# Optimization experiments

Hardware: AMD Instinct MI355X
Metric: run time of the kernel (lower is better)

## Reference

```python
import jax, jax.numpy as jnp
import numpy as np

B, T, DIN, DH, A = 2048, 32, 1024, 64, 64
EPS = 1e-12  # tf.contrib.layers.layer_norm variance epsilon


def _ln(x, g, b, axes):
    mu = jnp.mean(x, axes, keepdims=True)
    var = jnp.var(x, axes, keepdims=True)
    return (x - mu) / jnp.sqrt(var + EPS) * g + b


def _lstm(x_seq, W, b, H):
    # BasicLSTMCell: z = [x, h] @ W + b ; gates in order i, j, f, o ; forget_bias=1.0
    def step(carry, xt):
        c, h = carry
        z = jnp.concatenate([xt, h], axis=-1) @ W + b
        i, j, f, o = jnp.split(z, 4, axis=-1)
        c = c * jax.nn.sigmoid(f + 1.0) + jax.nn.sigmoid(i) * jnp.tanh(j)
        h = jnp.tanh(c) * jax.nn.sigmoid(o)
        return (c, h), h
    Bb = x_seq.shape[0]
    init = (jnp.zeros((Bb, H), x_seq.dtype), jnp.zeros((Bb, H), x_seq.dtype))
    _, hs = jax.lax.scan(step, init, jnp.swapaxes(x_seq, 0, 1))  # [T,B,H]
    return jnp.swapaxes(hs, 0, 1)  # [B,T,H]


def _revseq(x, lens):
    # tf.reverse_sequence along time axis 1
    t = jnp.arange(x.shape[1])[None, :]
    idx = jnp.where(t < lens[:, None], lens[:, None] - 1 - t, t)
    return jnp.take_along_axis(x, idx[:, :, None], axis=1)


def setup_inputs() -> dict:
    key = jax.random.key(0)
    ks = jax.random.split(key, 8)
    H = 512
    s_d = 1.0 / np.sqrt(DIN)
    s_l = 1.0 / np.sqrt(DH + H)
    return {
        "ud": jax.random.normal(ks[0], (B * T, DIN), jnp.float32),
        "mask": jnp.ones((B, T), jnp.float32),
        "au": jax.random.randint(ks[1], (B,), 1, T + 1, jnp.int32),
        "n_hidden": H,
        "ln1_g": jnp.ones((DIN,), jnp.float32),
        "ln1_b": jnp.zeros((DIN,), jnp.float32),
        "W_dense": jax.random.normal(ks[2], (DIN, DH), jnp.float32) * s_d,
        "b_dense": jnp.zeros((DH,), jnp.float32),
        "ln2_g": jnp.ones((DH,), jnp.float32),
        "ln2_b": jnp.zeros((DH,), jnp.float32),
        "W_fw": jax.random.normal(ks[3], (DH + H, 4 * H), jnp.float32) * s_l,
        "b_fw": jnp.zeros((4 * H,), jnp.float32),
        "W_bw": jax.random.normal(ks[4], (DH + H, 4 * H), jnp.float32) * s_l,
        "b_bw": jnp.zeros((4 * H,), jnp.float32),
        "ln3_g": jnp.ones((2 * H,), jnp.float32),
        "ln3_b": jnp.zeros((2 * H,), jnp.float32),
        "W_conv": jax.random.uniform(ks[5], (2 * H, A), jnp.float32, -0.003, 0.003),
        "b_conv": jnp.zeros((A,), jnp.float32),
    }


def reference(ud, mask, au, n_hidden, ln1_g, ln1_b, W_dense, b_dense, ln2_g, ln2_b,
              W_fw, b_fw, W_bw, b_bw, ln3_g, ln3_b, W_conv, b_conv):
    H = n_hidden
    x = _ln(ud, ln1_g, ln1_b, -1)                     # [B*T, DIN]
    x = x @ W_dense + b_dense                          # [B*T, DH]
    x = jax.nn.relu(_ln(x, ln2_g, ln2_b, -1))
    x = x.reshape(B, T, DH)
    tmask = (jnp.arange(T)[None, :] < au[:, None]).astype(x.dtype)  # [B,T]
    fw = _lstm(x, W_fw, b_fw, H) * tmask[:, :, None]
    bw = _revseq(_lstm(_revseq(x, au), W_bw, b_bw, H) * tmask[:, :, None], au)
    h = jnp.concatenate([fw, bw], axis=-1)             # [B,T,2H]
    # contrib layer_norm: begin_norm_axis=1 -> normalize over (T, 2H) jointly
    h = jax.nn.relu(_ln(h, ln3_g, ln3_b, (1, 2)))
    # conv1d kernel_size=stride=2H on [B, T*2H, 1] == per-timestep matmul
    out = jnp.tanh(jnp.einsum('bth,ha->bta', h, W_conv) + b_conv)  # [B,T,A]
    return out
```

## Files before the change

kernel.cpp:

```cpp
#include <hip/hip_runtime.h>

#define B_   2048
#define T_   32
#define DIN_ 1024
#define DH_  64
#define H_   512
#define KL_  576
#define AO_  64

typedef unsigned short u16;
typedef unsigned int   u32;
typedef __attribute__((ext_vector_type(8))) short          bf16x8;
typedef __attribute__((ext_vector_type(8))) unsigned short u16x8;
typedef __attribute__((ext_vector_type(4))) float          f32x4;

__device__ __forceinline__ u16 f2bf(float f) {
  u32 u = __builtin_bit_cast(u32, f);
  u = (u + 0x7FFFu + ((u >> 16) & 1u)) >> 16;
  return (u16)u;
}
__device__ __forceinline__ float bf2f(u16 s) {
  return __builtin_bit_cast(float, (u32)s << 16);
}
__device__ __forceinline__ float sigm(float x) { return 1.f / (1.f + __expf(-x)); }
__device__ __forceinline__ float tanh_(float x) { return 1.f - 2.f / (__expf(2.f * x) + 1.f); }

__device__ __forceinline__ void gl_lds16(const void* g, void* l) {
  __builtin_amdgcn_global_load_lds((const __attribute__((address_space(1))) u32*)g,
                                   (__attribute__((address_space(3))) u32*)l, 16, 0, 0);
}

__global__ __launch_bounds__(256) void k_transpose(const float* __restrict__ src,
                                                   u16* __restrict__ dst, int K, int N) {
  __shared__ float t[32][33];
  const int n0 = blockIdx.x * 32, k0 = blockIdx.y * 32;
  const int a = threadIdx.x >> 5, b = threadIdx.x & 31;
#pragma unroll
  for (int i = 0; i < 4; ++i)
    t[a + 8 * i][b] = src[(size_t)(k0 + a + 8 * i) * N + n0 + b];
  __syncthreads();
#pragma unroll
  for (int i = 0; i < 4; ++i)
    dst[(size_t)(n0 + a + 8 * i) * K + k0 + b] = f2bf(t[b][a + 8 * i]);
}

__global__ void k_gw(const float* __restrict__ W, const float* __restrict__ g,
                     const float* __restrict__ b, float* __restrict__ gW,
                     float* __restrict__ bW) {
  const int n = threadIdx.x;
  float sg = 0.f, sb = 0.f;
  for (int k = 0; k < DIN_; ++k) {
    const float w = W[k * DH_ + n];
    sg += g[k] * w; sb += b[k] * w;
  }
  gW[n] = sg; bW[n] = sb;
}

__global__ __launch_bounds__(256) void k_front(
    const float* __restrict__ ud, const float* __restrict__ g1,
    const u16* __restrict__ Wdt, const float* __restrict__ gW,
    const float* __restrict__ bW, const float* __restrict__ bd,
    const float* __restrict__ g2, const float* __restrict__ b2,
    u16* __restrict__ xout) {
  __shared__ u16 lA[64 * 32];
  __shared__ u16 lB[64 * 32];
  __shared__ float smu[64], srs[64];
  const int tid = threadIdx.x, wave = tid >> 6, lane = tid & 63;
  const int m0 = blockIdx.x * 64;
  const int arow = tid >> 2, ach = tid & 3;
  const float* __restrict__ udp = ud + (size_t)(m0 + arow) * DIN_ + ach * 8;
  const float* __restrict__ g1p = g1 + ach * 8;
  const int cB = wave * 16 + (lane >> 2);
  const u16* __restrict__ wdp = Wdt + (size_t)cB * DIN_ + (lane & 3) * 8;
  u16* const lBb = &lB[wave * 512];
  u16x8* const lAp = (u16x8*)&lA[arow * 32 + ach * 8];
  const int quad = lane >> 4, col = lane & 15;

  float sx = 0.f, sxx = 0.f;
  f32x4 acc[4] = {};
  for (int kt = 0; kt < 32; ++kt) {
    const int k0 = kt * 32;
    __syncthreads();
    const float4 v0 = *(const float4*)(udp + k0);
    const float4 v1 = *(const float4*)(udp + k0 + 4);
    const float4 ga = *(const float4*)(g1p + k0);
    const float4 gb = *(const float4*)(g1p + k0 + 4);
    sx  += v0.x + v0.y + v0.z + v0.w + v1.x + v1.y + v1.z + v1.w;
    sxx += v0.x * v0.x + v0.y * v0.y + v0.z * v0.z + v0.w * v0.w
         + v1.x * v1.x + v1.y * v1.y + v1.z * v1.z + v1.w * v1.w;
    u16x8 pk;
    pk[0] = f2bf(v0.x * ga.x); pk[1] = f2bf(v0.y * ga.y);
    pk[2] = f2bf(v0.z * ga.z); pk[3] = f2bf(v0.w * ga.w);
    pk[4] = f2bf(v1.x * gb.x); pk[5] = f2bf(v1.y * gb.y);
    pk[6] = f2bf(v1.z * gb.z); pk[7] = f2bf(v1.w * gb.w);
    *lAp = pk;
    gl_lds16(wdp + k0, lBb);
    __syncthreads();
    const bf16x8 af = *(const bf16x8*)&lA[(wave * 16 + col) * 32 + quad * 8];
#pragma unroll
    for (int nt = 0; nt < 4; ++nt) {
      const bf16x8 bfr = *(const bf16x8*)&lB[(nt * 16 + col) * 32 + quad * 8];
      acc[nt] = __builtin_amdgcn_mfma_f32_16x16x32_bf16(af, bfr, acc[nt], 0, 0, 0);
    }
  }
  sx  += __shfl_xor(sx, 1);  sx  += __shfl_xor(sx, 2);
  sxx += __shfl_xor(sxx, 1); sxx += __shfl_xor(sxx, 2);
  if ((lane & 3) == 0) {
    const float mu = sx * (1.f / DIN_);
    const float var = sxx * (1.f / DIN_) - mu * mu;
    smu[arow] = mu;
    srs[arow] = rsqrtf(var + 1e-12f);
  }
  __syncthreads();
  float gwv[4], bwv[4], g2v[4], b2v[4];
#pragma unroll
  for (int nt = 0; nt < 4; ++nt) {
    const int n = nt * 16 + col;
    gwv[nt] = gW[n]; bwv[nt] = bW[n] + bd[n]; g2v[nt] = g2[n]; b2v[nt] = b2[n];
  }
#pragma unroll
  for (int r = 0; r < 4; ++r) {
    const int rl = wave * 16 + quad * 4 + r;
    const float mu = smu[rl], rs = srs[rl];
    float y[4]; float s1 = 0.f, s2 = 0.f;
#pragma unroll
    for (int nt = 0; nt < 4; ++nt) {
      y[nt] = rs * (acc[nt][r] - mu * gwv[nt]) + bwv[nt];
      s1 += y[nt]; s2 += y[nt] * y[nt];
    }
    s1 += __shfl_xor(s1, 1); s1 += __shfl_xor(s1, 2);
    s1 += __shfl_xor(s1, 4); s1 += __shfl_xor(s1, 8);
    s2 += __shfl_xor(s2, 1); s2 += __shfl_xor(s2, 2);
    s2 += __shfl_xor(s2, 4); s2 += __shfl_xor(s2, 8);
    const float mu2 = s1 * (1.f / 64.f);
    const float rs2 = rsqrtf(s2 * (1.f / 64.f) - mu2 * mu2 + 1e-12f);
    const size_t R = m0 + rl;
#pragma unroll
    for (int nt = 0; nt < 4; ++nt) {
      const float v = fmaxf((y[nt] - mu2) * rs2 * g2v[nt] + b2v[nt], 0.f);
      xout[R * 64 + nt * 16 + col] = f2bf(v);
    }
  }
}

__global__ __launch_bounds__(256) void k_step(
    const int s, const u16* __restrict__ x, const u16* __restrict__ Wt,
    const float* __restrict__ bfw, const float* __restrict__ bbw,
    const int* __restrict__ au, u16* __restrict__ hstate,
    float* __restrict__ cstate, u16* __restrict__ hout) {
  __shared__ u16 lA[2][128 * 64];
  __shared__ u16 lB[2][128 * 64];
  const int tid = threadIdx.x, wave = tid >> 6, lane = tid & 63;
  const int dir = blockIdx.z;
  const int m0 = blockIdx.x * 128;
  const int u0 = blockIdx.y * 32;
  const int rb = s & 1, wb = rb ^ 1;
  const u16* __restrict__ Wtd = Wt + (size_t)dir * 2048 * KL_;
  const float* __restrict__ bias = dir ? bbw : bfw;

  const int lrow = lane >> 3;
  const int kk = ((lane & 7) ^ lrow) * 8;
  const int ch0 = 2 * wave, ch1 = ch0 + 1;

  const u16* gx[4]; const u16* gh[2]; const u16* gB[2];
#pragma unroll
  for (int i = 0; i < 2; ++i) {
    const int ch = ch0 + i;
#pragma unroll
    for (int h = 0; h < 2; ++h) {
      const int b = m0 + ch * 16 + h * 8 + lrow;
      const int aub = au[b];
      const int tin = (dir == 0) ? s : ((s < aub) ? (aub - 1 - s) : s);
      gx[i * 2 + h] = x + ((size_t)b * T_ + tin) * DH_ + kk;
    }
    const int b0 = m0 + ch * 16 + lrow;
    gh[i] = hstate + (((size_t)dir * 2 + rb) * B_ + b0) * H_ + kk;
    const int n = 512 * (ch & 3) + u0 + ((ch >> 2) << 4) + lrow;
    gB[i] = Wtd + (size_t)n * KL_ + kk;
  }

  gl_lds16(gx[0], &lA[0][ch0 * 1024]);
  gl_lds16(gx[1], &lA[0][ch0 * 1024 + 512]);
  gl_lds16(gx[2], &lA[0][ch1 * 1024]);
  gl_lds16(gx[3], &lA[0][ch1 * 1024 + 512]);
  gl_lds16(gB[0],           &lB[0][ch0 * 1024]);
  gl_lds16(gB[0] + 8 * KL_, &lB[0][ch0 * 1024 + 512]);
  gl_lds16(gB[1],           &lB[0][ch1 * 1024]);
  gl_lds16(gB[1] + 8 * KL_, &lB[0][ch1 * 1024 + 512]);
  __syncthreads();

  f32x4 acc[4][4] = {};
  const int wm = wave >> 1, wn = wave & 1, quad = lane >> 4, col = lane & 15;
  const int swz = (col & 7) << 4;

  int cur = 0;
  for (int kt = 0; kt < 9; ++kt) {
    if (kt < 8) {
      const int nb = cur ^ 1;
      const int kh = kt * 64;
      gl_lds16(gh[0] + kh,          &lA[nb][ch0 * 1024]);
      gl_lds16(gh[0] + kh + 8 * H_, &lA[nb][ch0 * 1024 + 512]);
      gl_lds16(gh[1] + kh,          &lA[nb][ch1 * 1024]);
      gl_lds16(gh[1] + kh + 8 * H_, &lA[nb][ch1 * 1024 + 512]);
      gl_lds16(gB[0] + kh + 64,            &lB[nb][ch0 * 1024]);
      gl_lds16(gB[0] + kh + 64 + 8 * KL_,  &lB[nb][ch0 * 1024 + 512]);
      gl_lds16(gB[1] + kh + 64,            &lB[nb][ch1 * 1024]);
      gl_lds16(gB[1] + kh + 64 + 8 * KL_,  &lB[nb][ch1 * 1024 + 512]);
    }
    const char* la = (const char*)&lA[cur][0];
    const char* lb = (const char*)&lB[cur][0];
#pragma unroll
    for (int ks = 0; ks < 2; ++ks) {
      const int bko = (ks * 64 + quad * 16) ^ swz;
      bf16x8 bfrag[4];
#pragma unroll
      for (int nt = 0; nt < 4; ++nt)
        bfrag[nt] = *(const bf16x8*)(lb + (wn * 64 + nt * 16 + col) * 128 + bko);
#pragma unroll
      for (int mt = 0; mt < 4; ++mt) {
        const bf16x8 afrag = *(const bf16x8*)(la + (wm * 64 + mt * 16 + col) * 128 + bko);
#pragma unroll
        for (int nt = 0; nt < 4; ++nt)
          acc[mt][nt] = __builtin_amdgcn_mfma_f32_16x16x32_bf16(afrag, bfrag[nt], acc[mt][nt], 0, 0, 0);
      }
    }
    __syncthreads();
    cur ^= 1;
  }

  const int u = u0 + wn * 16 + col;
  const float bi = bias[u], bj = bias[512 + u], bff = bias[1024 + u], bo = bias[1536 + u];
#pragma unroll
  for (int mt = 0; mt < 4; ++mt) {
#pragma unroll
    for (int r = 0; r < 4; ++r) {
      const int brow = m0 + wm * 64 + mt * 16 + quad * 4 + r;
      const size_t ci = ((size_t)dir * B_ + brow) * H_ + u;
      const float zi = acc[mt][0][r] + bi;
      const float zj = acc[mt][1][r] + bj;
      const float zf = acc[mt][2][r] + bff;
      const float zo = acc[mt][3][r] + bo;
      const float cn = cstate[ci] * sigm(zf + 1.f) + sigm(zi) * tanh_(zj);
      const float hn = tanh_(cn) * sigm(zo);
      cstate[ci] = cn;
      hstate[(((size_t)dir * 2 + wb) * B_ + brow) * H_ + u] = f2bf(hn);
      const int aub = au[brow];
      const bool valid = (s < aub);
      const int pos = (dir == 0) ? s : (valid ? (aub - 1 - s) : s);
      const float val = valid ? hn : 0.f;
      hout[((size_t)brow * T_ + pos) * 1024 + (dir ? 512 : 0) + u] = f2bf(val);
    }
  }
}

__global__ __launch_bounds__(256) void k_ln3stats(const u16* __restrict__ hout,
                                                  float* __restrict__ st) {
  const int b = blockIdx.x, tid = threadIdx.x;
  const uint4* __restrict__ p = (const uint4*)(hout + (size_t)b * T_ * 1024);
  float sx = 0.f, sxx = 0.f;
  for (int j = tid; j < 4096; j += 256) {
    const uint4 q = p[j];
    const u32 w[4] = {q.x, q.y, q.z, q.w};
#pragma unroll
    for (int e = 0; e < 4; ++e) {
      const float a = bf2f((u16)(w[e] & 0xffff));
      const float c = bf2f((u16)(w[e] >> 16));
      sx += a + c; sxx += a * a + c * c;
    }
  }
#pragma unroll
  for (int m = 1; m < 64; m <<= 1) { sx += __shfl_xor(sx, m); sxx += __shfl_xor(sxx, m); }
  __shared__ float rs_[4], rq_[4];
  if ((tid & 63) == 0) { rs_[tid >> 6] = sx; rq_[tid >> 6] = sxx; }
  __syncthreads();
  if (tid == 0) {
    const float a = rs_[0] + rs_[1] + rs_[2] + rs_[3];
    const float c = rq_[0] + rq_[1] + rq_[2] + rq_[3];
    const float mu = a / 32768.f;
    const float var = c / 32768.f - mu * mu;
    st[b * 2] = mu; st[b * 2 + 1] = rsqrtf(var + 1e-12f);
  }
}

__global__ __launch_bounds__(256) void k_final(
    const u16* __restrict__ hin, const float* __restrict__ st,
    const float* __restrict__ g3, const float* __restrict__ b3,
    const u16* __restrict__ Wct, const float* __restrict__ bc,
    float* __restrict__ out) {
  __shared__ u16 lA[64 * 32];
  __shared__ u16 lB[64 * 32];
  const int tid = threadIdx.x, wave = tid >> 6, lane = tid & 63;
  const int m0 = blockIdx.x * 64;
  const int arow = tid >> 2, ach = tid & 3;
  const size_t R = m0 + arow;
  const float mu = st[(R >> 5) * 2], rs = st[(R >> 5) * 2 + 1];
  const u16* __restrict__ hp = hin + R * 1024 + ach * 8;
  const float* __restrict__ g3p = g3 + ach * 8;
  const float* __restrict__ b3p = b3 + ach * 8;
  const int cB = wave * 16 + (lane >> 2);
  const u16* __restrict__ wcp = Wct + (size_t)cB * DIN_ + (lane & 3) * 8;
  u16* const lBb = &lB[wave * 512];
  u16x8* const lAp = (u16x8*)&lA[arow * 32 + ach * 8];
  const int quad = lane >> 4, col = lane & 15;
  f32x4 acc[4] = {};
  for (int kt = 0; kt < 32; ++kt) {
    const int k0 = kt * 32;
    __syncthreads();
    const uint4 q = *(const uint4*)(hp + k0);
    const float4 ga = *(const float4*)(g3p + k0);
    const float4 gb = *(const float4*)(g3p + k0 + 4);
    const float4 ba = *(const float4*)(b3p + k0);
    const float4 bb = *(const float4*)(b3p + k0 + 4);
    float hv[8];
    hv[0] = bf2f((u16)(q.x & 0xffff)); hv[1] = bf2f((u16)(q.x >> 16));
    hv[2] = bf2f((u16)(q.y & 0xffff)); hv[3] = bf2f((u16)(q.y >> 16));
    hv[4] = bf2f((u16)(q.z & 0xffff)); hv[5] = bf2f((u16)(q.z >> 16));
    hv[6] = bf2f((u16)(q.w & 0xffff)); hv[7] = bf2f((u16)(q.w >> 16));
    u16x8 pk;
    pk[0] = f2bf(fmaxf((hv[0] - mu) * rs * ga.x + ba.x, 0.f));
    pk[1] = f2bf(fmaxf((hv[1] - mu) * rs * ga.y + ba.y, 0.f));
    pk[2] = f2bf(fmaxf((hv[2] - mu) * rs * ga.z + ba.z, 0.f));
    pk[3] = f2bf(fmaxf((hv[3] - mu) * rs * ga.w + ba.w, 0.f));
    pk[4] = f2bf(fmaxf((hv[4] - mu) * rs * gb.x + bb.x, 0.f));
    pk[5] = f2bf(fmaxf((hv[5] - mu) * rs * gb.y + bb.y, 0.f));
    pk[6] = f2bf(fmaxf((hv[6] - mu) * rs * gb.z + bb.z, 0.f));
    pk[7] = f2bf(fmaxf((hv[7] - mu) * rs * gb.w + bb.w, 0.f));
    *lAp = pk;
    gl_lds16(wcp + k0, lBb);
    __syncthreads();
    const bf16x8 af = *(const bf16x8*)&lA[(wave * 16 + col) * 32 + quad * 8];
#pragma unroll
    for (int nt = 0; nt < 4; ++nt) {
      const bf16x8 bfr = *(const bf16x8*)&lB[(nt * 16 + col) * 32 + quad * 8];
      acc[nt] = __builtin_amdgcn_mfma_f32_16x16x32_bf16(af, bfr, acc[nt], 0, 0, 0);
    }
  }
  float bcv[4];
#pragma unroll
  for (int nt = 0; nt < 4; ++nt) bcv[nt] = bc[nt * 16 + col];
#pragma unroll
  for (int r = 0; r < 4; ++r) {
    const size_t R2 = m0 + wave * 16 + quad * 4 + r;
#pragma unroll
    for (int nt = 0; nt < 4; ++nt)
      out[R2 * 64 + nt * 16 + col] = tanh_(acc[nt][r] + bcv[nt]);
  }
}

extern "C" void kernel_launch(void* const* d_in, const int* in_sizes, int n_in,
                              void* d_out, int out_size, void* d_ws, size_t ws_size,
                              hipStream_t stream) {
  (void)in_sizes; (void)n_in; (void)out_size; (void)ws_size;
  const float* ud  = (const float*)d_in[0];
  const int*   au  = (const int*)d_in[2];
  const float* g1  = (const float*)d_in[4];
  const float* b1  = (const float*)d_in[5];
  const float* Wd  = (const float*)d_in[6];
  const float* bd  = (const float*)d_in[7];
  const float* g2  = (const float*)d_in[8];
  const float* b2  = (const float*)d_in[9];
  const float* Wfw = (const float*)d_in[10];
  const float* bfw = (const float*)d_in[11];
  const float* Wbw = (const float*)d_in[12];
  const float* bbw = (const float*)d_in[13];
  const float* g3  = (const float*)d_in[14];
  const float* b3  = (const float*)d_in[15];
  const float* Wc  = (const float*)d_in[16];
  const float* bc  = (const float*)d_in[17];

  char* p = (char*)d_ws;
  size_t off = 0;
  auto take = [&](size_t bytes) {
    char* r = p + off;
    off = (off + bytes + 255) & ~(size_t)255;
    return r;
  };
  u16*   xbf    = (u16*)  take((size_t)B_ * T_ * DH_ * 2);
  u16*   Wt     = (u16*)  take((size_t)2 * 2048 * KL_ * 2);
  u16*   Wdt    = (u16*)  take((size_t)DH_ * DIN_ * 2);
  u16*   Wct    = (u16*)  take((size_t)AO_ * DIN_ * 2);
  float* gWv    = (float*)take(64 * 4);
  float* bWv    = (float*)take(64 * 4);
  u16*   hstate = (u16*)  take((size_t)2 * 2 * B_ * H_ * 2);
  float* cstate = (float*)take((size_t)2 * B_ * H_ * 4);
  u16*   hout   = (u16*)  take((size_t)B_ * T_ * 1024 * 2);
  float* st3    = (float*)take((size_t)B_ * 2 * 4);

  hipMemsetAsync(hstate, 0, (size_t)2 * 2 * B_ * H_ * 2 + (size_t)2 * B_ * H_ * 4, stream);

  k_transpose<<<dim3(64, 18), 256, 0, stream>>>(Wfw, Wt,              KL_, 2048);
  k_transpose<<<dim3(64, 18), 256, 0, stream>>>(Wbw, Wt + 2048 * KL_, KL_, 2048);
  k_transpose<<<dim3(2, 32),  256, 0, stream>>>(Wd,  Wdt, DIN_, DH_);
  k_transpose<<<dim3(2, 32),  256, 0, stream>>>(Wc,  Wct, DIN_, AO_);
  k_gw<<<1, 64, 0, stream>>>(Wd, g1, b1, gWv, bWv);
  k_front<<<B_ * T_ / 64, 256, 0, stream>>>(ud, g1, Wdt, gWv, bWv, bd, g2, b2, xbf);
  for (int s = 0; s < T_; ++s)
    k_step<<<dim3(16, 16, 2), 256, 0, stream>>>(s, xbf, Wt, bfw, bbw, au, hstate, cstate, hout);
  k_ln3stats<<<B_, 256, 0, stream>>>(hout, st3);
  k_final<<<B_ * T_ / 64, 256, 0, stream>>>(hout, st3, g3, b3, Wct, bc, (float*)d_out);
}
```

Measured before the change: 1.234 ms.

## Fuse LSTM time steps into one persistent kernel with per-group barriers

```diff
diff --git a/kernel.cpp b/kernel.cpp
--- a/kernel.cpp
+++ b/kernel.cpp
@@ -30,6 +30,19 @@
                                    (__attribute__((address_space(3))) u32*)l, 16, 0, 0);
 }
 
+__device__ __forceinline__ void groupbar8(u32* c) {
+  __syncthreads();
+  if (threadIdx.x == 0) {
+    __threadfence();
+    const u32 t = __hip_atomic_fetch_add(c, 1u, __ATOMIC_RELEASE, __HIP_MEMORY_SCOPE_AGENT);
+    const u32 tgt = (t / 8u + 1u) * 8u;
+    while (__hip_atomic_load(c, __ATOMIC_RELAXED, __HIP_MEMORY_SCOPE_AGENT) < tgt)
+      __builtin_amdgcn_s_sleep(2);
+    __hip_atomic_fetch_add(c, 0u, __ATOMIC_ACQUIRE, __HIP_MEMORY_SCOPE_AGENT);
+  }
+  __syncthreads();
+}
+
 __global__ __launch_bounds__(256) void k_transpose(const float* __restrict__ src,
                                                    u16* __restrict__ dst, int K, int N) {
   __shared__ float t[32][33];
@@ -44,16 +57,24 @@
     dst[(size_t)(n0 + a + 8 * i) * K + k0 + b] = f2bf(t[b][a + 8 * i]);
 }
 
-__global__ void k_gw(const float* __restrict__ W, const float* __restrict__ g,
-                     const float* __restrict__ b, float* __restrict__ gW,
-                     float* __restrict__ bW) {
-  const int n = threadIdx.x;
+__global__ __launch_bounds__(256) void k_gw(const float* __restrict__ W, const float* __restrict__ g,
+                                            const float* __restrict__ b, float* __restrict__ gW,
+                                            float* __restrict__ bW) {
+  const int n = blockIdx.x, tid = threadIdx.x;
   float sg = 0.f, sb = 0.f;
-  for (int k = 0; k < DIN_; ++k) {
+  for (int k = tid; k < DIN_; k += 256) {
     const float w = W[k * DH_ + n];
     sg += g[k] * w; sb += b[k] * w;
   }
-  gW[n] = sg; bW[n] = sb;
+#pragma unroll
+  for (int m = 1; m < 64; m <<= 1) { sg += __shfl_xor(sg, m); sb += __shfl_xor(sb, m); }
+  __shared__ float r_[8];
+  if ((tid & 63) == 0) { r_[tid >> 6] = sg; r_[4 + (tid >> 6)] = sb; }
+  __syncthreads();
+  if (tid == 0) {
+    gW[n] = r_[0] + r_[1] + r_[2] + r_[3];
+    bW[n] = r_[4] + r_[5] + r_[6] + r_[7];
+  }
 }
 
 __global__ __launch_bounds__(256) void k_front(
@@ -143,113 +164,141 @@
   }
 }
 
-__global__ __launch_bounds__(256) void k_step(
-    const int s, const u16* __restrict__ x, const u16* __restrict__ Wt,
+__global__ __launch_bounds__(512, 2) void k_lstm(
+    const u16* __restrict__ x, const u16* __restrict__ Wt,
     const float* __restrict__ bfw, const float* __restrict__ bbw,
     const int* __restrict__ au, u16* __restrict__ hstate,
-    float* __restrict__ cstate, u16* __restrict__ hout) {
+    u16* __restrict__ hout, u32* __restrict__ bar) {
   __shared__ u16 lA[2][128 * 64];
-  __shared__ u16 lB[2][128 * 64];
+  __shared__ u16 lB[2][256 * 64];
   const int tid = threadIdx.x, wave = tid >> 6, lane = tid & 63;
-  const int dir = blockIdx.z;
-  const int m0 = blockIdx.x * 128;
-  const int u0 = blockIdx.y * 32;
-  const int rb = s & 1, wb = rb ^ 1;
+  const int bid = blockIdx.x;
+  const int grp = bid & 31;
+  const int dir = grp & 1;
+  const int m0 = (grp >> 1) * 128;
+  const int u0 = (bid >> 5) * 64;
+  u32* const gc = bar + grp * 32;
+
   const u16* __restrict__ Wtd = Wt + (size_t)dir * 2048 * KL_;
   const float* __restrict__ bias = dir ? bbw : bfw;
 
   const int lrow = lane >> 3;
   const int kk = ((lane & 7) ^ lrow) * 8;
-  const int ch0 = 2 * wave, ch1 = ch0 + 1;
-
-  const u16* gx[4]; const u16* gh[2]; const u16* gB[2];
+
+  const u16* xb[2]; int aux_[2];
+#pragma unroll
+  for (int h = 0; h < 2; ++h) {
+    const int b = m0 + wave * 16 + 8 * h + lrow;
+    aux_[h] = au[b];
+    xb[h] = x + (size_t)b * T_ * DH_ + kk;
+  }
+  const u16* const hbase = hstate + ((size_t)dir * 2 * B_ + m0 + wave * 16 + lrow) * H_ + kk;
+  const u16* gB[2];
 #pragma unroll
   for (int i = 0; i < 2; ++i) {
-    const int ch = ch0 + i;
-#pragma unroll
-    for (int h = 0; h < 2; ++h) {
-      const int b = m0 + ch * 16 + h * 8 + lrow;
-      const int aub = au[b];
-      const int tin = (dir == 0) ? s : ((s < aub) ? (aub - 1 - s) : s);
-      gx[i * 2 + h] = x + ((size_t)b * T_ + tin) * DH_ + kk;
-    }
-    const int b0 = m0 + ch * 16 + lrow;
-    gh[i] = hstate + (((size_t)dir * 2 + rb) * B_ + b0) * H_ + kk;
+    const int ch = 2 * wave + i;
     const int n = 512 * (ch & 3) + u0 + ((ch >> 2) << 4) + lrow;
     gB[i] = Wtd + (size_t)n * KL_ + kk;
   }
 
-  gl_lds16(gx[0], &lA[0][ch0 * 1024]);
-  gl_lds16(gx[1], &lA[0][ch0 * 1024 + 512]);
-  gl_lds16(gx[2], &lA[0][ch1 * 1024]);
-  gl_lds16(gx[3], &lA[0][ch1 * 1024 + 512]);
-  gl_lds16(gB[0],           &lB[0][ch0 * 1024]);
-  gl_lds16(gB[0] + 8 * KL_, &lB[0][ch0 * 1024 + 512]);
-  gl_lds16(gB[1],           &lB[0][ch1 * 1024]);
-  gl_lds16(gB[1] + 8 * KL_, &lB[0][ch1 * 1024 + 512]);
-  __syncthreads();
-
-  f32x4 acc[4][4] = {};
-  const int wm = wave >> 1, wn = wave & 1, quad = lane >> 4, col = lane & 15;
+  const int wm = wave >> 2, wn = wave & 3, quad = lane >> 4, col = lane & 15;
   const int swz = (col & 7) << 4;
-
-  int cur = 0;
-  for (int kt = 0; kt < 9; ++kt) {
-    if (kt < 8) {
-      const int nb = cur ^ 1;
-      const int kh = kt * 64;
-      gl_lds16(gh[0] + kh,          &lA[nb][ch0 * 1024]);
-      gl_lds16(gh[0] + kh + 8 * H_, &lA[nb][ch0 * 1024 + 512]);
-      gl_lds16(gh[1] + kh,          &lA[nb][ch1 * 1024]);
-      gl_lds16(gh[1] + kh + 8 * H_, &lA[nb][ch1 * 1024 + 512]);
-      gl_lds16(gB[0] + kh + 64,            &lB[nb][ch0 * 1024]);
-      gl_lds16(gB[0] + kh + 64 + 8 * KL_,  &lB[nb][ch0 * 1024 + 512]);
-      gl_lds16(gB[1] + kh + 64,            &lB[nb][ch1 * 1024]);
-      gl_lds16(gB[1] + kh + 64 + 8 * KL_,  &lB[nb][ch1 * 1024 + 512]);
-    }
-    const char* la = (const char*)&lA[cur][0];
-    const char* lb = (const char*)&lB[cur][0];
-#pragma unroll
-    for (int ks = 0; ks < 2; ++ks) {
-      const int bko = (ks * 64 + quad * 16) ^ swz;
-      bf16x8 bfrag[4];
-#pragma unroll
-      for (int nt = 0; nt < 4; ++nt)
-        bfrag[nt] = *(const bf16x8*)(lb + (wn * 64 + nt * 16 + col) * 128 + bko);
-#pragma unroll
-      for (int mt = 0; mt < 4; ++mt) {
-        const bf16x8 afrag = *(const bf16x8*)(la + (wm * 64 + mt * 16 + col) * 128 + bko);
-#pragma unroll
-        for (int nt = 0; nt < 4; ++nt)
-          acc[mt][nt] = __builtin_amdgcn_mfma_f32_16x16x32_bf16(afrag, bfrag[nt], acc[mt][nt], 0, 0, 0);
-      }
-    }
-    __syncthreads();
-    cur ^= 1;
-  }
-
   const int u = u0 + wn * 16 + col;
   const float bi = bias[u], bj = bias[512 + u], bff = bias[1024 + u], bo = bias[1536 + u];
-#pragma unroll
-  for (int mt = 0; mt < 4; ++mt) {
-#pragma unroll
-    for (int r = 0; r < 4; ++r) {
-      const int brow = m0 + wm * 64 + mt * 16 + quad * 4 + r;
-      const size_t ci = ((size_t)dir * B_ + brow) * H_ + u;
-      const float zi = acc[mt][0][r] + bi;
-      const float zj = acc[mt][1][r] + bj;
-      const float zf = acc[mt][2][r] + bff;
-      const float zo = acc[mt][3][r] + bo;
-      const float cn = cstate[ci] * sigm(zf + 1.f) + sigm(zi) * tanh_(zj);
-      const float hn = tanh_(cn) * sigm(zo);
-      cstate[ci] = cn;
-      hstate[(((size_t)dir * 2 + wb) * B_ + brow) * H_ + u] = f2bf(hn);
-      const int aub = au[brow];
-      const bool valid = (s < aub);
-      const int pos = (dir == 0) ? s : (valid ? (aub - 1 - s) : s);
-      const float val = valid ? hn : 0.f;
-      hout[((size_t)brow * T_ + pos) * 1024 + (dir ? 512 : 0) + u] = f2bf(val);
-    }
+  int aur[16];
+#pragma unroll
+  for (int mt = 0; mt < 4; ++mt)
+#pragma unroll
+    for (int r = 0; r < 4; ++r)
+      aur[mt * 4 + r] = au[m0 + wm * 64 + mt * 16 + quad * 4 + r];
+
+  float c[16];
+#pragma unroll
+  for (int i = 0; i < 16; ++i) c[i] = 0.f;
+
+  int cur = 0;
+  {
+#pragma unroll
+    for (int h = 0; h < 2; ++h) {
+      const int tin = (dir == 0) ? 0 : (aux_[h] - 1);
+      gl_lds16(xb[h] + tin * DH_, &lA[0][wave * 1024 + h * 512]);
+    }
+    gl_lds16(gB[0],           &lB[0][(2 * wave) * 1024]);
+    gl_lds16(gB[0] + 8 * KL_, &lB[0][(2 * wave) * 1024 + 512]);
+    gl_lds16(gB[1],           &lB[0][(2 * wave + 1) * 1024]);
+    gl_lds16(gB[1] + 8 * KL_, &lB[0][(2 * wave + 1) * 1024 + 512]);
+  }
+  __syncthreads();
+
+  for (int s = 0; s < T_; ++s) {
+    const int rb = s & 1, wb = rb ^ 1;
+    const u16* __restrict__ hb = hbase + (size_t)rb * B_ * H_;
+    f32x4 acc[4][4] = {};
+    for (int kt = 0; kt < 9; ++kt) {
+      if (kt < 8) {
+        const int nb = cur ^ 1;
+        const int kh = kt * 64;
+        gl_lds16(hb + kh,          &lA[nb][wave * 1024]);
+        gl_lds16(hb + kh + 8 * H_, &lA[nb][wave * 1024 + 512]);
+        gl_lds16(gB[0] + kh + 64,           &lB[nb][(2 * wave) * 1024]);
+        gl_lds16(gB[0] + kh + 64 + 8 * KL_, &lB[nb][(2 * wave) * 1024 + 512]);
+        gl_lds16(gB[1] + kh + 64,           &lB[nb][(2 * wave + 1) * 1024]);
+        gl_lds16(gB[1] + kh + 64 + 8 * KL_, &lB[nb][(2 * wave + 1) * 1024 + 512]);
+      }
+      const char* la = (const char*)&lA[cur][0];
+      const char* lb = (const char*)&lB[cur][0];
+#pragma unroll
+      for (int ks = 0; ks < 2; ++ks) {
+        const int bko = (ks * 64 + quad * 16) ^ swz;
+        bf16x8 bfrag[4];
+#pragma unroll
+        for (int nt = 0; nt < 4; ++nt)
+          bfrag[nt] = *(const bf16x8*)(lb + (wn * 64 + nt * 16 + col) * 128 + bko);
+#pragma unroll
+        for (int mt = 0; mt < 4; ++mt) {
+          const bf16x8 afrag = *(const bf16x8*)(la + (wm * 64 + mt * 16 + col) * 128 + bko);
+#pragma unroll
+          for (int nt = 0; nt < 4; ++nt)
+            acc[mt][nt] = __builtin_amdgcn_mfma_f32_16x16x32_bf16(afrag, bfrag[nt], acc[mt][nt], 0, 0, 0);
+        }
+      }
+      __syncthreads();
+      cur ^= 1;
+    }
+    if (s + 1 < T_) {
+      const int sn = s + 1;
+#pragma unroll
+      for (int h = 0; h < 2; ++h) {
+        const int aub = aux_[h];
+        const int tin = (dir == 0) ? sn : ((sn < aub) ? (aub - 1 - sn) : sn);
+        gl_lds16(xb[h] + tin * DH_, &lA[cur][wave * 1024 + h * 512]);
+      }
+      gl_lds16(gB[0],           &lB[cur][(2 * wave) * 1024]);
+      gl_lds16(gB[0] + 8 * KL_, &lB[cur][(2 * wave) * 1024 + 512]);
+      gl_lds16(gB[1],           &lB[cur][(2 * wave + 1) * 1024]);
+      gl_lds16(gB[1] + 8 * KL_, &lB[cur][(2 * wave + 1) * 1024 + 512]);
+    }
+#pragma unroll
+    for (int mt = 0; mt < 4; ++mt) {
+#pragma unroll
+      for (int r = 0; r < 4; ++r) {
+        const int brow = m0 + wm * 64 + mt * 16 + quad * 4 + r;
+        const float zi = acc[mt][0][r] + bi;
+        const float zj = acc[mt][1][r] + bj;
+        const float zf = acc[mt][2][r] + bff;
+        const float zo = acc[mt][3][r] + bo;
+        const float cn = c[mt * 4 + r] * sigm(zf + 1.f) + sigm(zi) * tanh_(zj);
+        const float hn = tanh_(cn) * sigm(zo);
+        c[mt * 4 + r] = cn;
+        hstate[(((size_t)dir * 2 + wb) * B_ + brow) * H_ + u] = f2bf(hn);
+        const int aub = aur[mt * 4 + r];
+        const bool valid = (s < aub);
+        const int pos = (dir == 0) ? s : (valid ? (aub - 1 - s) : s);
+        const float val = valid ? hn : 0.f;
+        hout[((size_t)brow * T_ + pos) * 1024 + (dir ? 512 : 0) + u] = f2bf(val);
+      }
+    }
+    if (s + 1 < T_) groupbar8(gc);
   }
 }
 
@@ -382,20 +431,21 @@
   float* gWv    = (float*)take(64 * 4);
   float* bWv    = (float*)take(64 * 4);
   u16*   hstate = (u16*)  take((size_t)2 * 2 * B_ * H_ * 2);
-  float* cstate = (float*)take((size_t)2 * B_ * H_ * 4);
+  u32*   barc   = (u32*)  take((size_t)32 * 32 * 4);
   u16*   hout   = (u16*)  take((size_t)B_ * T_ * 1024 * 2);
   float* st3    = (float*)take((size_t)B_ * 2 * 4);
 
-  hipMemsetAsync(hstate, 0, (size_t)2 * 2 * B_ * H_ * 2 + (size_t)2 * B_ * H_ * 4, stream);
+  hipMemsetAsync(hstate, 0, (size_t)2 * 2 * B_ * H_ * 2 + (size_t)32 * 32 * 4, stream);
 
   k_transpose<<<dim3(64, 18), 256, 0, stream>>>(Wfw, Wt,              KL_, 2048);
   k_transpose<<<dim3(64, 18), 256, 0, stream>>>(Wbw, Wt + 2048 * KL_, KL_, 2048);
   k_transpose<<<dim3(2, 32),  256, 0, stream>>>(Wd,  Wdt, DIN_, DH_);
   k_transpose<<<dim3(2, 32),  256, 0, stream>>>(Wc,  Wct, DIN_, AO_);
-  k_gw<<<1, 64, 0, stream>>>(Wd, g1, b1, gWv, bWv);
+  k_gw<<<64, 256, 0, stream>>>(Wd, g1, b1, gWv, bWv);
   k_front<<<B_ * T_ / 64, 256, 0, stream>>>(ud, g1, Wdt, gWv, bWv, bd, g2, b2, xbf);
-  for (int s = 0; s < T_; ++s)
-    k_step<<<dim3(16, 16, 2), 256, 0, stream>>>(s, xbf, Wt, bfw, bbw, au, hstate, cstate, hout);
+
+  k_lstm<<<dim3(256), dim3(512), 0, stream>>>(xbf, Wt, bfw, bbw, au, hstate, hout, barc);
+
   k_ln3stats<<<B_, 256, 0, stream>>>(hout, st3);
   k_final<<<B_ * T_ / 64, 256, 0, stream>>>(hout, st3, g3, b3, Wct, bc, (float*)d_out);
 }
```

New measurement: 1.547 ms. 25.3% more time.
